# Kernel optimization log

Hardware: AMD Instinct MI355X
Metric: run time of the kernel (lower is better)

The kernel has to match this reference:

```python
import jax, jax.numpy as jnp
import numpy as np

EMBED_DIM = 384
HIDDEN_DIM = 512
CODEBOOK_SIZE = 256
NUM_QUANTIZERS = 4
COMMIT_WEIGHT = 0.25
BATCH = 65536


def setup_inputs() -> dict:
    key = jax.random.key(0)
    ks = jax.random.split(key, 10)
    s_in = 1.0 / np.sqrt(EMBED_DIM)
    s_h = 1.0 / np.sqrt(HIDDEN_DIM)
    return {
        "x": jax.random.normal(ks[0], (BATCH, EMBED_DIM), jnp.float32),
        "enc_w1": jax.random.uniform(ks[1], (EMBED_DIM, HIDDEN_DIM), jnp.float32, -s_in, s_in),
        "enc_b1": jnp.zeros((HIDDEN_DIM,), jnp.float32),
        "enc_w2": jax.random.uniform(ks[2], (HIDDEN_DIM, HIDDEN_DIM), jnp.float32, -s_h, s_h),
        "enc_b2": jnp.zeros((HIDDEN_DIM,), jnp.float32),
        "codebooks": jax.random.normal(ks[3], (NUM_QUANTIZERS, CODEBOOK_SIZE, HIDDEN_DIM), jnp.float32),
        "dec_w1": jax.random.uniform(ks[4], (HIDDEN_DIM, HIDDEN_DIM), jnp.float32, -s_h, s_h),
        "dec_b1": jnp.zeros((HIDDEN_DIM,), jnp.float32),
        "dec_w2": jax.random.uniform(ks[5], (HIDDEN_DIM, EMBED_DIM), jnp.float32, -s_h, s_h),
        "dec_b2": jnp.zeros((EMBED_DIM,), jnp.float32),
    }


def _residual_vq(z, codebooks):
    """Sequential residual VQ with straight-through estimator and commitment loss.
    z: [B, D]; codebooks: [Q, K, D]. Returns quantized [B, D], indices [B, Q], commit_loss scalar."""
    residual = z
    quantized_out = jnp.zeros_like(z)
    commit_loss = jnp.asarray(0.0, z.dtype)
    idx_list = []
    for q in range(NUM_QUANTIZERS):
        cb = codebooks[q]  # [K, D]
        # nearest code: argmin ||r - c||^2 == argmax (2 r.c - ||c||^2)
        scores = 2.0 * (residual @ cb.T) - jnp.sum(cb * cb, axis=-1)  # [B, K]
        idx = jnp.argmax(scores, axis=-1)  # [B]
        quant = cb[idx]  # [B, D] gather
        commit_loss = commit_loss + COMMIT_WEIGHT * jnp.mean(
            (residual - jax.lax.stop_gradient(quant)) ** 2)
        # straight-through: value = quant, gradient flows to residual
        quant_st = residual + jax.lax.stop_gradient(quant - residual)
        quantized_out = quantized_out + quant_st
        residual = residual - jax.lax.stop_gradient(quant)
        idx_list.append(idx)
    indices = jnp.stack(idx_list, axis=-1)  # [B, Q]
    return quantized_out, indices, commit_loss


def reference(x, enc_w1, enc_b1, enc_w2, enc_b2, codebooks,
              dec_w1, dec_b1, dec_w2, dec_b2):
    # encoder MLP
    z = jax.nn.relu(x @ enc_w1 + enc_b1) @ enc_w2 + enc_b2  # [B, H]
    quantized, indices, commit_loss = _residual_vq(z, codebooks)
    # decoder MLP
    recon = jax.nn.relu(quantized @ dec_w1 + dec_b1) @ dec_w2 + dec_b2  # [B, E]
    recon_loss = jnp.mean((recon - x) ** 2)
    return recon, indices, recon_loss, commit_loss
```

## Files before the change

### kernel.cpp

```cpp
#include <hip/hip_runtime.h>
#include <cfloat>
#include <cstddef>


#define BATCH   65536
#define EDIM    384
#define HDIM    512
#define NCODE   256
#define NQ      4

#define OUT_IDX_OFF 25165824
#define OUT_RL_OFF  25427968
#define WS_BUFA     0
#define WS_BUFB     33554432
#define WS_CBSPL    67108864
#define WS_CNORM    67633152
#define WS_COMMITP  67634176
#define WS_RECONP   67636224
#define WS_W1S      67637760
#define WS_W2S      67834368
#define WS_W3S      68096512
#define WS_W4S      68358656

typedef _Float16 half8 __attribute__((ext_vector_type(8)));
typedef float    f32x16 __attribute__((ext_vector_type(16)));

__device__ __forceinline__ void cvt_hl(const float4& a0, const float4& a1,
                                       half8& h, half8& l)
{
    float vs[8] = {a0.x, a0.y, a0.z, a0.w, a1.x, a1.y, a1.z, a1.w};
#pragma unroll
    for (int j = 0; j < 8; ++j) {
        _Float16 hv = (_Float16)vs[j];
        h[j] = hv;
        l[j] = (_Float16)(vs[j] - (float)hv);
    }
}

__global__ __launch_bounds__(256)
void split_w(const float* __restrict__ W, unsigned short* __restrict__ out,
             int N, int K)
{
    int u = blockIdx.x * 256 + threadIdx.x;
    int col  = u % N;
    int rem  = u / N;
    int khalf = rem & 1;
    int kt    = rem >> 1;
    int kbase = kt * 16 + khalf * 8;
    half8 h, l;
#pragma unroll
    for (int j = 0; j < 8; ++j) {
        float v = W[(size_t)(kbase + j) * N + col];
        _Float16 hv = (_Float16)v;
        h[j] = hv;
        l[j] = (_Float16)(v - (float)hv);
    }
    size_t eh = ((size_t)(kt * 4 + khalf)) * N + col;
    size_t el = ((size_t)(kt * 4 + 2 + khalf)) * N + col;
    *reinterpret_cast<half8*>(out + eh * 8) = h;
    *reinterpret_cast<half8*>(out + el * 8) = l;
}

template <int BN, bool RELU, bool LOSS>
__global__ __launch_bounds__(256, 2)
void gemm_reg(const float* __restrict__ A, const unsigned short* __restrict__ Wsp,
              const float* __restrict__ bias, float* __restrict__ C,
              const float* __restrict__ X, float* __restrict__ lossP,
              int N, int K)
{
    constexpr int WN = BN / 128;
    constexpr int WM = 4 / WN;
    constexpr int MR = 128 / WM;
    constexpr int FM = MR / 32;

    const int tid  = threadIdx.x;
    const int wid  = tid >> 6;
    const int lane = tid & 63;
    const int l31  = lane & 31;
    const int lh   = lane >> 5;
    const int wm   = wid / WN;
    const int wn   = wid % WN;
    const int row0 = blockIdx.y * 128;
    const int n0   = blockIdx.x * BN;
    const int nkt  = K / 16;

    f32x16 acc[FM][4];
#pragma unroll
    for (int m = 0; m < FM; ++m)
#pragma unroll
        for (int n = 0; n < 4; ++n) acc[m][n] = (f32x16)(0.0f);

    const float* ap[FM];
#pragma unroll
    for (int fm = 0; fm < FM; ++fm)
        ap[fm] = A + (size_t)(row0 + wm * MR + fm * 32 + l31) * K + lh * 8;

    const half8* b8 = reinterpret_cast<const half8*>(Wsp);
    const int colb = n0 + wn * 128 + l31;

#pragma unroll 2
    for (int kt = 0; kt < nkt; ++kt) {
        half8 Ah[FM], Al[FM];
#pragma unroll
        for (int fm = 0; fm < FM; ++fm) {
            float4 a0 = *reinterpret_cast<const float4*>(ap[fm] + kt * 16);
            float4 a1 = *reinterpret_cast<const float4*>(ap[fm] + kt * 16 + 4);
            cvt_hl(a0, a1, Ah[fm], Al[fm]);
        }
        const size_t eh = (size_t)(kt * 4 + lh) * N + colb;
        const size_t el = (size_t)(kt * 4 + 2 + lh) * N + colb;
#pragma unroll
        for (int nt = 0; nt < 4; ++nt) {
            half8 Bh = b8[eh + nt * 32];
            half8 Bl = b8[el + nt * 32];
#pragma unroll
            for (int fm = 0; fm < FM; ++fm) {
                acc[fm][nt] = __builtin_amdgcn_mfma_f32_32x32x16_f16(Ah[fm], Bh, acc[fm][nt], 0, 0, 0);
                acc[fm][nt] = __builtin_amdgcn_mfma_f32_32x32x16_f16(Ah[fm], Bl, acc[fm][nt], 0, 0, 0);
                acc[fm][nt] = __builtin_amdgcn_mfma_f32_32x32x16_f16(Al[fm], Bh, acc[fm][nt], 0, 0, 0);
            }
        }
    }

    float lacc = 0.f;
#pragma unroll
    for (int fm = 0; fm < FM; ++fm) {
#pragma unroll
        for (int nt = 0; nt < 4; ++nt) {
            const int col = n0 + wn * 128 + nt * 32 + l31;
            const float b = bias[col];
#pragma unroll
            for (int rg = 0; rg < 16; ++rg) {
                const int row = row0 + wm * MR + fm * 32 + (rg & 3) + 8 * (rg >> 2) + 4 * lh;
                float v = acc[fm][nt][rg] + b;
                if (RELU) v = v > 0.f ? v : 0.f;
                C[(size_t)row * N + col] = v;
                if constexpr (LOSS) {
                    float d = v - X[(size_t)row * N + col];
                    lacc = fmaf(d, d, lacc);
                }
            }
        }
    }

    if constexpr (LOSS) {
        __shared__ float red[256];
        red[tid] = lacc;
        __syncthreads();
        for (int s = 128; s > 0; s >>= 1) {
            if (tid < s) red[tid] += red[tid + s];
            __syncthreads();
        }
        if (tid == 0) lossP[blockIdx.y * gridDim.x + blockIdx.x] = red[0];
    }
}

__global__ __launch_bounds__(64)
void cnorm_kernel(const float* __restrict__ cb, float* __restrict__ cnorm)
{
    const int code = blockIdx.x;
    const int lane = threadIdx.x;
    const float* r = cb + (size_t)code * HDIM;
    float s = 0.f;
    for (int k = lane; k < HDIM; k += 64) s = fmaf(r[k], r[k], s);
#pragma unroll
    for (int off = 32; off > 0; off >>= 1) s += __shfl_down(s, off);
    if (lane == 0) cnorm[code] = s;
}

__global__ __launch_bounds__(256)
void split_cb(const float* __restrict__ cb, unsigned short* __restrict__ out)
{
    int u = blockIdx.x * 256 + threadIdx.x;
    int q    = u >> 14;
    int rem  = u & 16383;
    int code = rem >> 6;
    int kt   = (rem >> 1) & 31;
    int khalf = rem & 1;
    int k = kt * 16 + khalf * 8;
    const float* p = cb + ((size_t)(q * NCODE + code)) * HDIM + k;
    float4 v0 = *reinterpret_cast<const float4*>(p);
    float4 v1 = *reinterpret_cast<const float4*>(p + 4);
    half8 h, l;
    cvt_hl(v0, v1, h, l);
    size_t o = (size_t)(q * 32 + kt) * 8192 + (size_t)khalf * 2048 + (size_t)code * 8;
    *reinterpret_cast<half8*>(out + o)        = h;
    *reinterpret_cast<half8*>(out + o + 4096) = l;
}

template <bool LAST>
__global__ __launch_bounds__(256, 2)
void vq_stage(int q,
              const float* __restrict__ Rin, float* __restrict__ Rout,
              const float* __restrict__ zsrc,
              const unsigned short* __restrict__ cbs,
              const float* __restrict__ cb,
              const float* __restrict__ cnorm,
              float* __restrict__ idx_out,
              float* __restrict__ commitP)
{
    __shared__ float sval[2][128];
    __shared__ int   sidx[2][128];
    __shared__ int   idxbuf[128];
    __shared__ float red[256];

    const int tid  = threadIdx.x;
    const int wid  = tid >> 6;
    const int lane = tid & 63;
    const int l31  = lane & 31;
    const int lh   = lane >> 5;
    const int wm   = wid >> 1;
    const int wn   = wid & 1;
    const int row0 = blockIdx.x * 128;

    f32x16 acc[2][4];
#pragma unroll
    for (int m = 0; m < 2; ++m)
#pragma unroll
        for (int n = 0; n < 4; ++n) acc[m][n] = (f32x16)(0.0f);

    const float* ap[2];
#pragma unroll
    for (int fm = 0; fm < 2; ++fm)
        ap[fm] = Rin + (size_t)(row0 + wm * 64 + fm * 32 + l31) * HDIM + lh * 8;

    const half8* c8 = reinterpret_cast<const half8*>(cbs);
    const size_t qbase = (size_t)q * 32 * 1024;
    const int code_b = wn * 128 + l31;

#pragma unroll 4
    for (int kt = 0; kt < 32; ++kt) {
        half8 Ah[2], Al[2];
#pragma unroll
        for (int fm = 0; fm < 2; ++fm) {
            float4 a0 = *reinterpret_cast<const float4*>(ap[fm] + kt * 16);
            float4 a1 = *reinterpret_cast<const float4*>(ap[fm] + kt * 16 + 4);
            cvt_hl(a0, a1, Ah[fm], Al[fm]);
        }
        const size_t eh = qbase + (size_t)kt * 1024 + (size_t)lh * 256 + code_b;
#pragma unroll
        for (int nt = 0; nt < 4; ++nt) {
            half8 Bh = c8[eh + nt * 32];
            half8 Bl = c8[eh + 512 + nt * 32];
#pragma unroll
            for (int fm = 0; fm < 2; ++fm) {
                acc[fm][nt] = __builtin_amdgcn_mfma_f32_32x32x16_f16(Ah[fm], Bh, acc[fm][nt], 0, 0, 0);
                acc[fm][nt] = __builtin_amdgcn_mfma_f32_32x32x16_f16(Ah[fm], Bl, acc[fm][nt], 0, 0, 0);
                acc[fm][nt] = __builtin_amdgcn_mfma_f32_32x32x16_f16(Al[fm], Bh, acc[fm][nt], 0, 0, 0);
            }
        }
    }

    const float* cn = cnorm + q * NCODE;
#pragma unroll
    for (int Mt = 0; Mt < 2; ++Mt) {
#pragma unroll
        for (int rg = 0; rg < 16; ++rg) {
            float bv = -FLT_MAX;
            int   bi = 0;
#pragma unroll
            for (int nt = 0; nt < 4; ++nt) {
                const int code = wn * 128 + nt * 32 + l31;
                float s = 2.f * acc[Mt][nt][rg] - cn[code];
                if (s > bv || (s == bv && code < bi)) { bv = s; bi = code; }
            }
#pragma unroll
            for (int m = 1; m < 32; m <<= 1) {
                float ov = __shfl_xor(bv, m, 64);
                int   oi = __shfl_xor(bi, m, 64);
                if (ov > bv || (ov == bv && oi < bi)) { bv = ov; bi = oi; }
            }
            if (l31 == 0) {
                int row = wm * 64 + Mt * 32 + (rg & 3) + 8 * (rg >> 2) + 4 * lh;
                sval[wn][row] = bv;
                sidx[wn][row] = bi;
            }
        }
    }
    __syncthreads();
    if (tid < 128) {
        float v0 = sval[0][tid], v1 = sval[1][tid];
        int   i0 = sidx[0][tid], i1 = sidx[1][tid];
        int b = (v1 > v0 || (v1 == v0 && i1 < i0)) ? i1 : i0;
        idxbuf[tid] = b;
        idx_out[(size_t)(row0 + tid) * NQ + q] = (float)b;
    }
    __syncthreads();

    float ca = 0.f;
    const int rgrp = tid >> 3;
    const int lpos = tid & 7;
#pragma unroll
    for (int rr = 0; rr < 4; ++rr) {
        const int row = rr * 32 + rgrp;
        const float* rin  = Rin + (size_t)(row0 + row) * HDIM;
        const float* crow = cb + ((size_t)q * NCODE + idxbuf[row]) * HDIM;
        float* rout = Rout + (size_t)(row0 + row) * HDIM;
        const float* zr = LAST ? (zsrc + (size_t)(row0 + row) * HDIM) : nullptr;
#pragma unroll
        for (int j = 0; j < 16; ++j) {
            const int f4 = lpos + j * 8;
            float4 rv = *reinterpret_cast<const float4*>(rin + f4 * 4);
            float4 cv = *reinterpret_cast<const float4*>(crow + f4 * 4);
            float4 d;
            d.x = rv.x - cv.x; d.y = rv.y - cv.y;
            d.z = rv.z - cv.z; d.w = rv.w - cv.w;
            ca = fmaf(d.x, d.x, ca); ca = fmaf(d.y, d.y, ca);
            ca = fmaf(d.z, d.z, ca); ca = fmaf(d.w, d.w, ca);
            if constexpr (LAST) {
                float4 zv = *reinterpret_cast<const float4*>(zr + f4 * 4);
                float4 qv;
                qv.x = zv.x - d.x; qv.y = zv.y - d.y;
                qv.z = zv.z - d.z; qv.w = zv.w - d.w;
                *reinterpret_cast<float4*>(rout + f4 * 4) = qv;
            } else {
                *reinterpret_cast<float4*>(rout + f4 * 4) = d;
            }
        }
    }

    red[tid] = ca;
    __syncthreads();
    for (int s = 128; s > 0; s >>= 1) {
        if (tid < s) red[tid] += red[tid + s];
        __syncthreads();
    }
    if (tid == 0) commitP[q * 512 + blockIdx.x] = red[0];
}

__global__ __launch_bounds__(256)
void loss_reduce(const float* __restrict__ cP, int nc,
                 const float* __restrict__ rP, int nr,
                 float* __restrict__ out2)
{
    __shared__ float red[256];
    const int tid = threadIdx.x;

    float s = 0.f;
    for (int i = tid; i < nc; i += 256) s += cP[i];
    red[tid] = s;
    __syncthreads();
    for (int st = 128; st > 0; st >>= 1) {
        if (tid < st) red[tid] += red[tid + st];
        __syncthreads();
    }
    float ctot = red[0];
    __syncthreads();

    s = 0.f;
    for (int i = tid; i < nr; i += 256) s += rP[i];
    red[tid] = s;
    __syncthreads();
    for (int st = 128; st > 0; st >>= 1) {
        if (tid < st) red[tid] += red[tid + st];
        __syncthreads();
    }
    if (tid == 0) {
        out2[0] = red[0] / ((float)BATCH * (float)EDIM);
        out2[1] = 0.25f * ctot / ((float)BATCH * (float)HDIM);
    }
}

extern "C" void kernel_launch(void* const* d_in, const int* in_sizes, int n_in,
                              void* d_out, int out_size, void* d_ws, size_t ws_size,
                              hipStream_t stream)
{
    const float* x   = (const float*)d_in[0];
    const float* ew1 = (const float*)d_in[1];
    const float* eb1 = (const float*)d_in[2];
    const float* ew2 = (const float*)d_in[3];
    const float* eb2 = (const float*)d_in[4];
    const float* cb  = (const float*)d_in[5];
    const float* dw1 = (const float*)d_in[6];
    const float* db1 = (const float*)d_in[7];
    const float* dw2 = (const float*)d_in[8];
    const float* db2 = (const float*)d_in[9];

    float* out  = (float*)d_out;
    float* ws   = (float*)d_ws;
    float* bufA = ws + WS_BUFA;
    float* bufB = ws + WS_BUFB;
    unsigned short* cbs = (unsigned short*)(ws + WS_CBSPL);
    float* cn   = ws + WS_CNORM;
    float* cP   = ws + WS_COMMITP;
    float* rP   = ws + WS_RECONP;
    unsigned short* w1s = (unsigned short*)(ws + WS_W1S);
    unsigned short* w2s = (unsigned short*)(ws + WS_W2S);
    unsigned short* w3s = (unsigned short*)(ws + WS_W3S);
    unsigned short* w4s = (unsigned short*)(ws + WS_W4S);

    cnorm_kernel<<<NQ * NCODE, 64, 0, stream>>>(cb, cn);
    split_cb<<<256, 256, 0, stream>>>(cb, cbs);
    split_w<<<(EDIM / 16) * 2 * HDIM / 256, 256, 0, stream>>>(ew1, w1s, HDIM, EDIM);
    split_w<<<(HDIM / 16) * 2 * HDIM / 256, 256, 0, stream>>>(ew2, w2s, HDIM, HDIM);
    split_w<<<(HDIM / 16) * 2 * HDIM / 256, 256, 0, stream>>>(dw1, w3s, HDIM, HDIM);
    split_w<<<(HDIM / 16) * 2 * EDIM / 256, 256, 0, stream>>>(dw2, w4s, EDIM, HDIM);

    gemm_reg<256, true, false><<<dim3(HDIM / 256, BATCH / 128), 256, 0, stream>>>(
        x, w1s, eb1, bufA, nullptr, nullptr, HDIM, EDIM);
    gemm_reg<256, false, false><<<dim3(HDIM / 256, BATCH / 128), 256, 0, stream>>>(
        bufA, w2s, eb2, bufB, nullptr, nullptr, HDIM, HDIM);

    float* idxo = out + OUT_IDX_OFF;
    vq_stage<false><<<512, 256, 0, stream>>>(0, bufB, bufA, nullptr, cbs, cb, cn, idxo, cP);
    vq_stage<false><<<512, 256, 0, stream>>>(1, bufA, bufA, nullptr, cbs, cb, cn, idxo, cP);
    vq_stage<false><<<512, 256, 0, stream>>>(2, bufA, bufA, nullptr, cbs, cb, cn, idxo, cP);
    vq_stage<true ><<<512, 256, 0, stream>>>(3, bufA, bufB, bufB,    cbs, cb, cn, idxo, cP);

    gemm_reg<256, true, false><<<dim3(HDIM / 256, BATCH / 128), 256, 0, stream>>>(
        bufB, w3s, db1, bufA, nullptr, nullptr, HDIM, HDIM);
    gemm_reg<128, false, true><<<dim3(EDIM / 128, BATCH / 128), 256, 0, stream>>>(
        bufA, w4s, db2, out, x, rP, EDIM, HDIM);

    loss_reduce<<<1, 256, 0, stream>>>(cP, NQ * 512, rP,
                                       (BATCH / 128) * (EDIM / 128),
                                       out + OUT_RL_OFF);
}
```

Baseline: 1.046 ms.

## Software-pipeline register prefetch of A and B tiles in GEMM and VQ kernels

Adds a register-level multi-stage prefetch to the GEMM and VQ-score kernels. A operands are loaded three k-steps ahead and B operands two k-steps ahead, with the K loop fully unrolled through a compile-time trip count. This is meant to hide global-memory latency behind the MFMA work. The extra buffers raise register pressure, so launch bounds drop to one block per SIMD, which lowers occupancy.

```diff
diff --git a/kernel.cpp b/kernel.cpp
--- a/kernel.cpp
+++ b/kernel.cpp
@@ -61,17 +61,20 @@
     *reinterpret_cast<half8*>(out + el * 8) = l;
 }
 
-template <int BN, bool RELU, bool LOSS>
-__global__ __launch_bounds__(256, 2)
+template <int BN, int NKT, bool RELU, bool LOSS>
+__global__ __launch_bounds__(256, 1)
 void gemm_reg(const float* __restrict__ A, const unsigned short* __restrict__ Wsp,
               const float* __restrict__ bias, float* __restrict__ C,
               const float* __restrict__ X, float* __restrict__ lossP,
-              int N, int K)
+              int N)
 {
     constexpr int WN = BN / 128;
     constexpr int WM = 4 / WN;
     constexpr int MR = 128 / WM;
     constexpr int FM = MR / 32;
+    constexpr int K  = NKT * 16;
+    constexpr int DA = 3;
+    constexpr int DB = 2;
 
     const int tid  = threadIdx.x;
     const int wid  = tid >> 6;
@@ -82,7 +85,6 @@
     const int wn   = wid % WN;
     const int row0 = blockIdx.y * 128;
     const int n0   = blockIdx.x * BN;
-    const int nkt  = K / 16;
 
     f32x16 acc[FM][4];
 #pragma unroll
@@ -98,28 +100,63 @@
     const half8* b8 = reinterpret_cast<const half8*>(Wsp);
     const int colb = n0 + wn * 128 + l31;
 
-#pragma unroll 2
-    for (int kt = 0; kt < nkt; ++kt) {
+    float4 ar0[DA][FM], ar1[DA][FM];
+    half8  brh[DB][4], brl[DB][4];
+
+#pragma unroll
+    for (int p = 0; p < DA; ++p)
+#pragma unroll
+        for (int fm = 0; fm < FM; ++fm) {
+            ar0[p][fm] = *reinterpret_cast<const float4*>(ap[fm] + p * 16);
+            ar1[p][fm] = *reinterpret_cast<const float4*>(ap[fm] + p * 16 + 4);
+        }
+#pragma unroll
+    for (int p = 0; p < DB; ++p) {
+        const size_t eh = (size_t)(p * 4 + lh) * N + colb;
+        const size_t el = (size_t)(p * 4 + 2 + lh) * N + colb;
+#pragma unroll
+        for (int nt = 0; nt < 4; ++nt) {
+            brh[p][nt] = b8[eh + nt * 32];
+            brl[p][nt] = b8[el + nt * 32];
+        }
+    }
+
+#pragma unroll
+    for (int kt = 0; kt < NKT; ++kt) {
+        const int sa = kt % DA;
+        const int sb = kt % DB;
+
         half8 Ah[FM], Al[FM];
 #pragma unroll
-        for (int fm = 0; fm < FM; ++fm) {
-            float4 a0 = *reinterpret_cast<const float4*>(ap[fm] + kt * 16);
-            float4 a1 = *reinterpret_cast<const float4*>(ap[fm] + kt * 16 + 4);
-            cvt_hl(a0, a1, Ah[fm], Al[fm]);
-        }
-        const size_t eh = (size_t)(kt * 4 + lh) * N + colb;
-        const size_t el = (size_t)(kt * 4 + 2 + lh) * N + colb;
-#pragma unroll
-        for (int nt = 0; nt < 4; ++nt) {
-            half8 Bh = b8[eh + nt * 32];
-            half8 Bl = b8[el + nt * 32];
+        for (int fm = 0; fm < FM; ++fm)
+            cvt_hl(ar0[sa][fm], ar1[sa][fm], Ah[fm], Al[fm]);
+        if (kt + DA < NKT) {
 #pragma unroll
             for (int fm = 0; fm < FM; ++fm) {
-                acc[fm][nt] = __builtin_amdgcn_mfma_f32_32x32x16_f16(Ah[fm], Bh, acc[fm][nt], 0, 0, 0);
-                acc[fm][nt] = __builtin_amdgcn_mfma_f32_32x32x16_f16(Ah[fm], Bl, acc[fm][nt], 0, 0, 0);
-                acc[fm][nt] = __builtin_amdgcn_mfma_f32_32x32x16_f16(Al[fm], Bh, acc[fm][nt], 0, 0, 0);
-            }
-        }
+                ar0[sa][fm] = *reinterpret_cast<const float4*>(ap[fm] + (kt + DA) * 16);
+                ar1[sa][fm] = *reinterpret_cast<const float4*>(ap[fm] + (kt + DA) * 16 + 4);
+            }
+        }
+        half8 Bh[4], Bl[4];
+#pragma unroll
+        for (int nt = 0; nt < 4; ++nt) { Bh[nt] = brh[sb][nt]; Bl[nt] = brl[sb][nt]; }
+        if (kt + DB < NKT) {
+            const size_t eh = (size_t)((kt + DB) * 4 + lh) * N + colb;
+            const size_t el = (size_t)((kt + DB) * 4 + 2 + lh) * N + colb;
+#pragma unroll
+            for (int nt = 0; nt < 4; ++nt) {
+                brh[sb][nt] = b8[eh + nt * 32];
+                brl[sb][nt] = b8[el + nt * 32];
+            }
+        }
+#pragma unroll
+        for (int nt = 0; nt < 4; ++nt)
+#pragma unroll
+            for (int fm = 0; fm < FM; ++fm) {
+                acc[fm][nt] = __builtin_amdgcn_mfma_f32_32x32x16_f16(Ah[fm], Bh[nt], acc[fm][nt], 0, 0, 0);
+                acc[fm][nt] = __builtin_amdgcn_mfma_f32_32x32x16_f16(Ah[fm], Bl[nt], acc[fm][nt], 0, 0, 0);
+                acc[fm][nt] = __builtin_amdgcn_mfma_f32_32x32x16_f16(Al[fm], Bh[nt], acc[fm][nt], 0, 0, 0);
+            }
     }
 
     float lacc = 0.f;
@@ -189,7 +226,7 @@
 }
 
 template <bool LAST>
-__global__ __launch_bounds__(256, 2)
+__global__ __launch_bounds__(256, 1)
 void vq_stage(int q,
               const float* __restrict__ Rin, float* __restrict__ Rout,
               const float* __restrict__ zsrc,
@@ -199,6 +236,10 @@
               float* __restrict__ idx_out,
               float* __restrict__ commitP)
 {
+    constexpr int DA = 3;
+    constexpr int DB = 2;
+    constexpr int NKT = 32;
+
     __shared__ float sval[2][128];
     __shared__ int   sidx[2][128];
     __shared__ int   idxbuf[128];
@@ -228,27 +269,61 @@
     const size_t qbase = (size_t)q * 32 * 1024;
     const int code_b = wn * 128 + l31;
 
-#pragma unroll 4
-    for (int kt = 0; kt < 32; ++kt) {
+    float4 ar0[DA][2], ar1[DA][2];
+    half8  brh[DB][4], brl[DB][4];
+
+#pragma unroll
+    for (int p = 0; p < DA; ++p)
+#pragma unroll
+        for (int fm = 0; fm < 2; ++fm) {
+            ar0[p][fm] = *reinterpret_cast<const float4*>(ap[fm] + p * 16);
+            ar1[p][fm] = *reinterpret_cast<const float4*>(ap[fm] + p * 16 + 4);
+        }
+#pragma unroll
+    for (int p = 0; p < DB; ++p) {
+        const size_t eh = qbase + (size_t)p * 1024 + (size_t)lh * 256 + code_b;
+#pragma unroll
+        for (int nt = 0; nt < 4; ++nt) {
+            brh[p][nt] = c8[eh + nt * 32];
+            brl[p][nt] = c8[eh + 512 + nt * 32];
+        }
+    }
+
+#pragma unroll
+    for (int kt = 0; kt < NKT; ++kt) {
+        const int sa = kt % DA;
+        const int sb = kt % DB;
+
         half8 Ah[2], Al[2];
 #pragma unroll
-        for (int fm = 0; fm < 2; ++fm) {
-            float4 a0 = *reinterpret_cast<const float4*>(ap[fm] + kt * 16);
-            float4 a1 = *reinterpret_cast<const float4*>(ap[fm] + kt * 16 + 4);
-            cvt_hl(a0, a1, Ah[fm], Al[fm]);
-        }
-        const size_t eh = qbase + (size_t)kt * 1024 + (size_t)lh * 256 + code_b;
-#pragma unroll
-        for (int nt = 0; nt < 4; ++nt) {
-            half8 Bh = c8[eh + nt * 32];
-            half8 Bl = c8[eh + 512 + nt * 32];
+        for (int fm = 0; fm < 2; ++fm)
+            cvt_hl(ar0[sa][fm], ar1[sa][fm], Ah[fm], Al[fm]);
+        if (kt + DA < NKT) {
 #pragma unroll
             for (int fm = 0; fm < 2; ++fm) {
-                acc[fm][nt] = __builtin_amdgcn_mfma_f32_32x32x16_f16(Ah[fm], Bh, acc[fm][nt], 0, 0, 0);
-                acc[fm][nt] = __builtin_amdgcn_mfma_f32_32x32x16_f16(Ah[fm], Bl, acc[fm][nt], 0, 0, 0);
-                acc[fm][nt] = __builtin_amdgcn_mfma_f32_32x32x16_f16(Al[fm], Bh, acc[fm][nt], 0, 0, 0);
-            }
-        }
+                ar0[sa][fm] = *reinterpret_cast<const float4*>(ap[fm] + (kt + DA) * 16);
+                ar1[sa][fm] = *reinterpret_cast<const float4*>(ap[fm] + (kt + DA) * 16 + 4);
+            }
+        }
+        half8 Bh[4], Bl[4];
+#pragma unroll
+        for (int nt = 0; nt < 4; ++nt) { Bh[nt] = brh[sb][nt]; Bl[nt] = brl[sb][nt]; }
+        if (kt + DB < NKT) {
+            const size_t eh = qbase + (size_t)(kt + DB) * 1024 + (size_t)lh * 256 + code_b;
+#pragma unroll
+            for (int nt = 0; nt < 4; ++nt) {
+                brh[sb][nt] = c8[eh + nt * 32];
+                brl[sb][nt] = c8[eh + 512 + nt * 32];
+            }
+        }
+#pragma unroll
+        for (int nt = 0; nt < 4; ++nt)
+#pragma unroll
+            for (int fm = 0; fm < 2; ++fm) {
+                acc[fm][nt] = __builtin_amdgcn_mfma_f32_32x32x16_f16(Ah[fm], Bh[nt], acc[fm][nt], 0, 0, 0);
+                acc[fm][nt] = __builtin_amdgcn_mfma_f32_32x32x16_f16(Ah[fm], Bl[nt], acc[fm][nt], 0, 0, 0);
+                acc[fm][nt] = __builtin_amdgcn_mfma_f32_32x32x16_f16(Al[fm], Bh[nt], acc[fm][nt], 0, 0, 0);
+            }
     }
 
     const float* cn = cnorm + q * NCODE;
@@ -396,10 +471,10 @@
     split_w<<<(HDIM / 16) * 2 * HDIM / 256, 256, 0, stream>>>(dw1, w3s, HDIM, HDIM);
     split_w<<<(HDIM / 16) * 2 * EDIM / 256, 256, 0, stream>>>(dw2, w4s, EDIM, HDIM);
 
-    gemm_reg<256, true, false><<<dim3(HDIM / 256, BATCH / 128), 256, 0, stream>>>(
-        x, w1s, eb1, bufA, nullptr, nullptr, HDIM, EDIM);
-    gemm_reg<256, false, false><<<dim3(HDIM / 256, BATCH / 128), 256, 0, stream>>>(
-        bufA, w2s, eb2, bufB, nullptr, nullptr, HDIM, HDIM);
+    gemm_reg<256, 24, true, false><<<dim3(HDIM / 256, BATCH / 128), 256, 0, stream>>>(
+        x, w1s, eb1, bufA, nullptr, nullptr, HDIM);
+    gemm_reg<256, 32, false, false><<<dim3(HDIM / 256, BATCH / 128), 256, 0, stream>>>(
+        bufA, w2s, eb2, bufB, nullptr, nullptr, HDIM);
 
     float* idxo = out + OUT_IDX_OFF;
     vq_stage<false><<<512, 256, 0, stream>>>(0, bufB, bufA, nullptr, cbs, cb, cn, idxo, cP);
@@ -407,10 +482,10 @@
     vq_stage<false><<<512, 256, 0, stream>>>(2, bufA, bufA, nullptr, cbs, cb, cn, idxo, cP);
     vq_stage<true ><<<512, 256, 0, stream>>>(3, bufA, bufB, bufB,    cbs, cb, cn, idxo, cP);
 
-    gemm_reg<256, true, false><<<dim3(HDIM / 256, BATCH / 128), 256, 0, stream>>>(
-        bufB, w3s, db1, bufA, nullptr, nullptr, HDIM, HDIM);
-    gemm_reg<128, false, true><<<dim3(EDIM / 128, BATCH / 128), 256, 0, stream>>>(
-        bufA, w4s, db2, out, x, rP, EDIM, HDIM);
+    gemm_reg<256, 32, true, false><<<dim3(HDIM / 256, BATCH / 128), 256, 0, stream>>>(
+        bufB, w3s, db1, bufA, nullptr, nullptr, HDIM);
+    gemm_reg<128, 32, false, true><<<dim3(EDIM / 128, BATCH / 128), 256, 0, stream>>>(
+        bufA, w4s, db2, out, x, rP, EDIM);
 
     loss_reduce<<<1, 256, 0, stream>>>(cP, NQ * 512, rP,
                                        (BATCH / 128) * (EDIM / 128),
```

Measured after the change: 1.220 ms. 1.17x slower.

## Pipeline GEMM and VQ tiles through LDS with pre-split fp16 hi/lo activations

Applied to the files above, without the earlier changes.

Replaces direct global loads in the GEMM and VQ kernels with a three-buffer LDS pipeline filled by global_load_lds, using manual vmcnt waits and raw barriers. Intermediate activations are now stored already split into fp16 hi/lo pairs in a k-tiled layout, and a new split_x kernel pre-splits the input x. The aim is to hide global memory latency and to stop every output-column block from redoing the fp32-to-fp16 split of the same activations. The cost is an extra pass over x and hand-written wait counts and buffer indexing that must match exactly, plus LDS use that may lower occupancy.

```diff
diff --git a/kernel.cpp b/kernel.cpp
--- a/kernel.cpp
+++ b/kernel.cpp
@@ -1,6 +1,7 @@
 #include <hip/hip_runtime.h>
 #include <cfloat>
 #include <cstddef>
+#include <cstdint>
 
 
 #define BATCH   65536
@@ -11,8 +12,8 @@
 
 #define OUT_IDX_OFF 25165824
 #define OUT_RL_OFF  25427968
-#define WS_BUFA     0
-#define WS_BUFB     33554432
+#define WS_P0       0
+#define WS_P1       33554432
 #define WS_CBSPL    67108864
 #define WS_CNORM    67633152
 #define WS_COMMITP  67634176
@@ -25,16 +26,53 @@
 typedef _Float16 half8 __attribute__((ext_vector_type(8)));
 typedef float    f32x16 __attribute__((ext_vector_type(16)));
 
-__device__ __forceinline__ void cvt_hl(const float4& a0, const float4& a1,
-                                       half8& h, half8& l)
-{
-    float vs[8] = {a0.x, a0.y, a0.z, a0.w, a1.x, a1.y, a1.z, a1.w};
+__device__ __forceinline__ void cvt_hl8(const float* vs, half8& h, half8& l)
+{
 #pragma unroll
     for (int j = 0; j < 8; ++j) {
         _Float16 hv = (_Float16)vs[j];
         h[j] = hv;
         l[j] = (_Float16)(vs[j] - (float)hv);
     }
+}
+
+__device__ __forceinline__ void gll16(const unsigned short* g, unsigned short* l)
+{
+    __builtin_amdgcn_global_load_lds(
+        (const __attribute__((address_space(1))) unsigned int*)g,
+        (__attribute__((address_space(3))) unsigned int*)l, 16, 0, 0);
+}
+
+template <int N> __device__ __forceinline__ void waitvm()
+{
+    __builtin_amdgcn_sched_barrier(0);
+    if constexpr (N == 0)      asm volatile("s_waitcnt vmcnt(0)" ::: "memory");
+    else if constexpr (N == 4) asm volatile("s_waitcnt vmcnt(4)" ::: "memory");
+    else if constexpr (N == 6) asm volatile("s_waitcnt vmcnt(6)" ::: "memory");
+    __builtin_amdgcn_sched_barrier(0);
+}
+__device__ __forceinline__ void barrier_raw()
+{
+    __builtin_amdgcn_s_barrier();
+    __builtin_amdgcn_sched_barrier(0);
+}
+
+__global__ __launch_bounds__(256)
+void split_x(const float* __restrict__ x, unsigned short* __restrict__ xs)
+{
+    int u = blockIdx.x * 256 + threadIdx.x;
+    int row = u / 48;
+    int rem = u % 48;
+    int kt = rem >> 1, khalf = rem & 1;
+    const float* p = x + (size_t)row * EDIM + kt * 16 + khalf * 8;
+    float vs[8];
+#pragma unroll
+    for (int j = 0; j < 8; ++j) vs[j] = p[j];
+    half8 h, l;
+    cvt_hl8(vs, h, l);
+    unsigned short* o = xs + (size_t)row * 768 + kt * 32 + khalf * 8;
+    *reinterpret_cast<half8*>(o)      = h;
+    *reinterpret_cast<half8*>(o + 16) = l;
 }
 
 __global__ __launch_bounds__(256)
@@ -47,31 +85,67 @@
     int khalf = rem & 1;
     int kt    = rem >> 1;
     int kbase = kt * 16 + khalf * 8;
+    float vs[8];
+#pragma unroll
+    for (int j = 0; j < 8; ++j) vs[j] = W[(size_t)(kbase + j) * N + col];
     half8 h, l;
-#pragma unroll
-    for (int j = 0; j < 8; ++j) {
-        float v = W[(size_t)(kbase + j) * N + col];
-        _Float16 hv = (_Float16)v;
-        h[j] = hv;
-        l[j] = (_Float16)(v - (float)hv);
-    }
-    size_t eh = ((size_t)(kt * 4 + khalf)) * N + col;
-    size_t el = ((size_t)(kt * 4 + 2 + khalf)) * N + col;
-    *reinterpret_cast<half8*>(out + eh * 8) = h;
-    *reinterpret_cast<half8*>(out + el * 8) = l;
-}
-
-template <int BN, bool RELU, bool LOSS>
+    cvt_hl8(vs, h, l);
+    *reinterpret_cast<half8*>(out + ((size_t)(kt * 4 + khalf) * N + col) * 8)     = h;
+    *reinterpret_cast<half8*>(out + ((size_t)(kt * 4 + 2 + khalf) * N + col) * 8) = l;
+}
+
+__global__ __launch_bounds__(256)
+void split_cb(const float* __restrict__ cb, unsigned short* __restrict__ out)
+{
+    int u = blockIdx.x * 256 + threadIdx.x;
+    int q    = u >> 14;
+    int rem  = u & 16383;
+    int code = rem >> 6;
+    int kt   = (rem >> 1) & 31;
+    int khalf = rem & 1;
+    int k = kt * 16 + khalf * 8;
+    const float* p = cb + ((size_t)(q * NCODE + code)) * HDIM + k;
+    float vs[8];
+#pragma unroll
+    for (int j = 0; j < 8; ++j) vs[j] = p[j];
+    half8 h, l;
+    cvt_hl8(vs, h, l);
+    size_t o = (size_t)(q * 32 + kt) * 8192 + (size_t)khalf * 2048 + (size_t)code * 8;
+    *reinterpret_cast<half8*>(out + o)        = h;
+    *reinterpret_cast<half8*>(out + o + 4096) = l;
+}
+
+__global__ __launch_bounds__(64)
+void cnorm_kernel(const float* __restrict__ cb, float* __restrict__ cnorm)
+{
+    const int code = blockIdx.x;
+    const int lane = threadIdx.x;
+    const float* r = cb + (size_t)code * HDIM;
+    float s = 0.f;
+    for (int k = lane; k < HDIM; k += 64) s = fmaf(r[k], r[k], s);
+#pragma unroll
+    for (int off = 32; off > 0; off >>= 1) s += __shfl_down(s, off);
+    if (lane == 0) cnorm[code] = s;
+}
+
+template <int BN, int NKT, int OMODE, bool RELU>
 __global__ __launch_bounds__(256, 2)
-void gemm_reg(const float* __restrict__ A, const unsigned short* __restrict__ Wsp,
-              const float* __restrict__ bias, float* __restrict__ C,
-              const float* __restrict__ X, float* __restrict__ lossP,
-              int N, int K)
-{
-    constexpr int WN = BN / 128;
-    constexpr int WM = 4 / WN;
-    constexpr int MR = 128 / WM;
-    constexpr int FM = MR / 32;
+void gemm_pl(const unsigned short* __restrict__ Ain,
+             const unsigned short* __restrict__ Wsp,
+             const float* __restrict__ bias, void* __restrict__ Cout,
+             const float* __restrict__ X, float* __restrict__ lossP, int N)
+{
+    constexpr int WN  = BN / 128;
+    constexpr int WM  = 4 / WN;
+    constexpr int MR  = 128 / WM;
+    constexpr int FM  = MR / 32;
+    constexpr int K   = NKT * 16;
+    constexpr int BOFF = 4096;
+    constexpr int BUFU = 4096 + 4 * BN * 8;
+    constexpr int NIB = BN / 64;
+    constexpr int GPI = 2 + NIB;
+
+    __shared__ __align__(16) unsigned short lds[3][BUFU];
 
     const int tid  = threadIdx.x;
     const int wid  = tid >> 6;
@@ -82,7 +156,6 @@
     const int wn   = wid % WN;
     const int row0 = blockIdx.y * 128;
     const int n0   = blockIdx.x * BN;
-    const int nkt  = K / 16;
 
     f32x16 acc[FM][4];
 #pragma unroll
@@ -90,29 +163,42 @@
 #pragma unroll
         for (int n = 0; n < 4; ++n) acc[m][n] = (f32x16)(0.0f);
 
-    const float* ap[FM];
-#pragma unroll
-    for (int fm = 0; fm < FM; ++fm)
-        ap[fm] = A + (size_t)(row0 + wm * MR + fm * 32 + l31) * K + lh * 8;
-
-    const half8* b8 = reinterpret_cast<const half8*>(Wsp);
-    const int colb = n0 + wn * 128 + l31;
-
-#pragma unroll 2
-    for (int kt = 0; kt < nkt; ++kt) {
+    auto stageB = [&](int buf, int kt) {
+        const unsigned short* img = Wsp + (size_t)kt * 4 * N * 8;
+        unsigned short* dstb = &lds[buf][BOFF];
+#pragma unroll
+        for (int t = 0; t < NIB; ++t) {
+            int e = (wid * NIB + t) * 64 + lane;
+            int u = (BN == 256) ? (e >> 8) : (e >> 7);
+            int c = e & (BN - 1);
+            gll16(img + ((size_t)u * N + n0 + c) * 8, dstb + (size_t)e * 8);
+        }
+    };
+    auto stageA = [&](int buf, int kt) {
+#pragma unroll
+        for (int t = 0; t < 2; ++t) {
+            int i = wid * 2 + t;
+            int u = i >> 1, rh = i & 1;
+            int row = rh * 64 + lane;
+            gll16(Ain + (size_t)(row0 + row) * (2 * K) + kt * 32 + u * 8,
+                  &lds[buf][(size_t)i * 512 + (size_t)lane * 8]);
+        }
+    };
+    auto compute = [&](int buf) {
+        const unsigned short* Ab = &lds[buf][0];
+        const unsigned short* Bb = &lds[buf][BOFF];
         half8 Ah[FM], Al[FM];
 #pragma unroll
         for (int fm = 0; fm < FM; ++fm) {
-            float4 a0 = *reinterpret_cast<const float4*>(ap[fm] + kt * 16);
-            float4 a1 = *reinterpret_cast<const float4*>(ap[fm] + kt * 16 + 4);
-            cvt_hl(a0, a1, Ah[fm], Al[fm]);
-        }
-        const size_t eh = (size_t)(kt * 4 + lh) * N + colb;
-        const size_t el = (size_t)(kt * 4 + 2 + lh) * N + colb;
+            int row = wm * MR + fm * 32 + l31;
+            Ah[fm] = *reinterpret_cast<const half8*>(Ab + (size_t)lh * 1024 + (size_t)row * 8);
+            Al[fm] = *reinterpret_cast<const half8*>(Ab + (size_t)(2 + lh) * 1024 + (size_t)row * 8);
+        }
 #pragma unroll
         for (int nt = 0; nt < 4; ++nt) {
-            half8 Bh = b8[eh + nt * 32];
-            half8 Bl = b8[el + nt * 32];
+            int col = wn * 128 + nt * 32 + l31;
+            half8 Bh = *reinterpret_cast<const half8*>(Bb + (size_t)lh * BN * 8 + (size_t)col * 8);
+            half8 Bl = *reinterpret_cast<const half8*>(Bb + (size_t)(2 + lh) * BN * 8 + (size_t)col * 8);
 #pragma unroll
             for (int fm = 0; fm < FM; ++fm) {
                 acc[fm][nt] = __builtin_amdgcn_mfma_f32_32x32x16_f16(Ah[fm], Bh, acc[fm][nt], 0, 0, 0);
@@ -120,30 +206,64 @@
                 acc[fm][nt] = __builtin_amdgcn_mfma_f32_32x32x16_f16(Al[fm], Bh, acc[fm][nt], 0, 0, 0);
             }
         }
-    }
-
-    float lacc = 0.f;
-#pragma unroll
-    for (int fm = 0; fm < FM; ++fm) {
-#pragma unroll
-        for (int nt = 0; nt < 4; ++nt) {
-            const int col = n0 + wn * 128 + nt * 32 + l31;
-            const float b = bias[col];
-#pragma unroll
-            for (int rg = 0; rg < 16; ++rg) {
-                const int row = row0 + wm * MR + fm * 32 + (rg & 3) + 8 * (rg >> 2) + 4 * lh;
-                float v = acc[fm][nt][rg] + b;
-                if (RELU) v = v > 0.f ? v : 0.f;
-                C[(size_t)row * N + col] = v;
-                if constexpr (LOSS) {
+    };
+
+    stageA(0, 0); stageB(0, 0);
+    stageA(1, 1); stageB(1, 1);
+    waitvm<GPI>();
+    barrier_raw();
+    for (int kt = 0; kt < NKT; ++kt) {
+        const int cur = kt % 3;
+        if (kt + 2 < NKT) { const int nb = (kt + 2) % 3; stageA(nb, kt + 2); stageB(nb, kt + 2); }
+        compute(cur);
+        if (kt < NKT - 2) waitvm<GPI>(); else waitvm<0>();
+        barrier_raw();
+    }
+
+    if constexpr (OMODE == 0) {
+        unsigned short* o = (unsigned short*)Cout;
+        const size_t rs = (size_t)N * 2;
+#pragma unroll
+        for (int fm = 0; fm < FM; ++fm) {
+#pragma unroll
+            for (int nt = 0; nt < 4; ++nt) {
+                const int col = n0 + wn * 128 + nt * 32 + l31;
+                const float b = bias[col];
+                const size_t cbo = (size_t)(col >> 4) * 32 + (size_t)((col >> 3) & 1) * 8 + (col & 7);
+#pragma unroll
+                for (int rg = 0; rg < 16; ++rg) {
+                    const int row = row0 + wm * MR + fm * 32 + (rg & 3) + 8 * (rg >> 2) + 4 * lh;
+                    float v = acc[fm][nt][rg] + b;
+                    if (RELU) v = v > 0.f ? v : 0.f;
+                    _Float16 hv = (_Float16)v;
+                    _Float16 lv = (_Float16)(v - (float)hv);
+                    union { _Float16 f; unsigned short u; } ch, cl;
+                    ch.f = hv; cl.f = lv;
+                    o[(size_t)row * rs + cbo]      = ch.u;
+                    o[(size_t)row * rs + cbo + 16] = cl.u;
+                }
+            }
+        }
+    } else {
+        float* C = (float*)Cout;
+        float lacc = 0.f;
+#pragma unroll
+        for (int fm = 0; fm < FM; ++fm) {
+#pragma unroll
+            for (int nt = 0; nt < 4; ++nt) {
+                const int col = n0 + wn * 128 + nt * 32 + l31;
+                const float b = bias[col];
+#pragma unroll
+                for (int rg = 0; rg < 16; ++rg) {
+                    const int row = row0 + wm * MR + fm * 32 + (rg & 3) + 8 * (rg >> 2) + 4 * lh;
+                    float v = acc[fm][nt][rg] + b;
+                    if (RELU) v = v > 0.f ? v : 0.f;
+                    C[(size_t)row * N + col] = v;
                     float d = v - X[(size_t)row * N + col];
                     lacc = fmaf(d, d, lacc);
                 }
             }
         }
-    }
-
-    if constexpr (LOSS) {
         __shared__ float red[256];
         red[tid] = lacc;
         __syncthreads();
@@ -155,50 +275,19 @@
     }
 }
 
-__global__ __launch_bounds__(64)
-void cnorm_kernel(const float* __restrict__ cb, float* __restrict__ cnorm)
-{
-    const int code = blockIdx.x;
-    const int lane = threadIdx.x;
-    const float* r = cb + (size_t)code * HDIM;
-    float s = 0.f;
-    for (int k = lane; k < HDIM; k += 64) s = fmaf(r[k], r[k], s);
-#pragma unroll
-    for (int off = 32; off > 0; off >>= 1) s += __shfl_down(s, off);
-    if (lane == 0) cnorm[code] = s;
-}
-
-__global__ __launch_bounds__(256)
-void split_cb(const float* __restrict__ cb, unsigned short* __restrict__ out)
-{
-    int u = blockIdx.x * 256 + threadIdx.x;
-    int q    = u >> 14;
-    int rem  = u & 16383;
-    int code = rem >> 6;
-    int kt   = (rem >> 1) & 31;
-    int khalf = rem & 1;
-    int k = kt * 16 + khalf * 8;
-    const float* p = cb + ((size_t)(q * NCODE + code)) * HDIM + k;
-    float4 v0 = *reinterpret_cast<const float4*>(p);
-    float4 v1 = *reinterpret_cast<const float4*>(p + 4);
-    half8 h, l;
-    cvt_hl(v0, v1, h, l);
-    size_t o = (size_t)(q * 32 + kt) * 8192 + (size_t)khalf * 2048 + (size_t)code * 8;
-    *reinterpret_cast<half8*>(out + o)        = h;
-    *reinterpret_cast<half8*>(out + o + 4096) = l;
-}
-
 template <bool LAST>
 __global__ __launch_bounds__(256, 2)
 void vq_stage(int q,
-              const float* __restrict__ Rin, float* __restrict__ Rout,
-              const float* __restrict__ zsrc,
+              const unsigned short* __restrict__ Rin, unsigned short* __restrict__ Rout,
+              const unsigned short* __restrict__ zsrc,
               const unsigned short* __restrict__ cbs,
               const float* __restrict__ cb,
               const float* __restrict__ cnorm,
               float* __restrict__ idx_out,
               float* __restrict__ commitP)
 {
+    constexpr int NKT = 32;
+    __shared__ __align__(16) unsigned short lds[3][12288];
     __shared__ float sval[2][128];
     __shared__ int   sidx[2][128];
     __shared__ int   idxbuf[128];
@@ -219,29 +308,40 @@
 #pragma unroll
         for (int n = 0; n < 4; ++n) acc[m][n] = (f32x16)(0.0f);
 
-    const float* ap[2];
-#pragma unroll
-    for (int fm = 0; fm < 2; ++fm)
-        ap[fm] = Rin + (size_t)(row0 + wm * 64 + fm * 32 + l31) * HDIM + lh * 8;
-
-    const half8* c8 = reinterpret_cast<const half8*>(cbs);
-    const size_t qbase = (size_t)q * 32 * 1024;
-    const int code_b = wn * 128 + l31;
-
-#pragma unroll 4
-    for (int kt = 0; kt < 32; ++kt) {
+    auto stageA = [&](int buf, int kt) {
+#pragma unroll
+        for (int t = 0; t < 2; ++t) {
+            int i = wid * 2 + t;
+            int u = i >> 1, rh = i & 1;
+            int row = rh * 64 + lane;
+            gll16(Rin + (size_t)(row0 + row) * 1024 + kt * 32 + u * 8,
+                  &lds[buf][(size_t)i * 512 + (size_t)lane * 8]);
+        }
+    };
+    auto stageB = [&](int buf, int kt) {
+        const unsigned short* img = cbs + (size_t)(q * 32 + kt) * 8192;
+        unsigned short* dstb = &lds[buf][4096];
+#pragma unroll
+        for (int t = 0; t < 4; ++t) {
+            int e = (wid * 4 + t) * 64 + lane;
+            gll16(img + (size_t)e * 8, dstb + (size_t)e * 8);
+        }
+    };
+    auto compute = [&](int buf) {
+        const unsigned short* Ab = &lds[buf][0];
+        const unsigned short* Bb = &lds[buf][4096];
         half8 Ah[2], Al[2];
 #pragma unroll
         for (int fm = 0; fm < 2; ++fm) {
-            float4 a0 = *reinterpret_cast<const float4*>(ap[fm] + kt * 16);
-            float4 a1 = *reinterpret_cast<const float4*>(ap[fm] + kt * 16 + 4);
-            cvt_hl(a0, a1, Ah[fm], Al[fm]);
-        }
-        const size_t eh = qbase + (size_t)kt * 1024 + (size_t)lh * 256 + code_b;
+            int row = wm * 64 + fm * 32 + l31;
+            Ah[fm] = *reinterpret_cast<const half8*>(Ab + (size_t)lh * 1024 + (size_t)row * 8);
+            Al[fm] = *reinterpret_cast<const half8*>(Ab + (size_t)(2 + lh) * 1024 + (size_t)row * 8);
+        }
 #pragma unroll
         for (int nt = 0; nt < 4; ++nt) {
-            half8 Bh = c8[eh + nt * 32];
-            half8 Bl = c8[eh + 512 + nt * 32];
+            int col = wn * 128 + nt * 32 + l31;
+            half8 Bh = *reinterpret_cast<const half8*>(Bb + (size_t)lh * 2048 + (size_t)col * 8);
+            half8 Bl = *reinterpret_cast<const half8*>(Bb + (size_t)(2 + lh) * 2048 + (size_t)col * 8);
 #pragma unroll
             for (int fm = 0; fm < 2; ++fm) {
                 acc[fm][nt] = __builtin_amdgcn_mfma_f32_32x32x16_f16(Ah[fm], Bh, acc[fm][nt], 0, 0, 0);
@@ -249,6 +349,18 @@
                 acc[fm][nt] = __builtin_amdgcn_mfma_f32_32x32x16_f16(Al[fm], Bh, acc[fm][nt], 0, 0, 0);
             }
         }
+    };
+
+    stageA(0, 0); stageB(0, 0);
+    stageA(1, 1); stageB(1, 1);
+    waitvm<6>();
+    barrier_raw();
+    for (int kt = 0; kt < NKT; ++kt) {
+        const int cur = kt % 3;
+        if (kt + 2 < NKT) { const int nb = (kt + 2) % 3; stageA(nb, kt + 2); stageB(nb, kt + 2); }
+        compute(cur);
+        if (kt < NKT - 2) waitvm<6>(); else waitvm<0>();
+        barrier_raw();
     }
 
     const float* cn = cnorm + q * NCODE;
@@ -293,29 +405,41 @@
 #pragma unroll
     for (int rr = 0; rr < 4; ++rr) {
         const int row = rr * 32 + rgrp;
-        const float* rin  = Rin + (size_t)(row0 + row) * HDIM;
+        const unsigned short* rip = Rin + (size_t)(row0 + row) * 1024;
+        unsigned short*       rop = Rout + (size_t)(row0 + row) * 1024;
         const float* crow = cb + ((size_t)q * NCODE + idxbuf[row]) * HDIM;
-        float* rout = Rout + (size_t)(row0 + row) * HDIM;
-        const float* zr = LAST ? (zsrc + (size_t)(row0 + row) * HDIM) : nullptr;
-#pragma unroll
-        for (int j = 0; j < 16; ++j) {
-            const int f4 = lpos + j * 8;
-            float4 rv = *reinterpret_cast<const float4*>(rin + f4 * 4);
-            float4 cv = *reinterpret_cast<const float4*>(crow + f4 * 4);
-            float4 d;
-            d.x = rv.x - cv.x; d.y = rv.y - cv.y;
-            d.z = rv.z - cv.z; d.w = rv.w - cv.w;
-            ca = fmaf(d.x, d.x, ca); ca = fmaf(d.y, d.y, ca);
-            ca = fmaf(d.z, d.z, ca); ca = fmaf(d.w, d.w, ca);
+        const unsigned short* zp = LAST ? (zsrc + (size_t)(row0 + row) * 1024) : nullptr;
+#pragma unroll
+        for (int j = 0; j < 8; ++j) {
+            const int g = lpos + j * 8;
+            const size_t off = (size_t)(g >> 1) * 32 + (size_t)(g & 1) * 8;
+            half8 rh = *reinterpret_cast<const half8*>(rip + off);
+            half8 rl = *reinterpret_cast<const half8*>(rip + off + 16);
+            float4 c0 = *reinterpret_cast<const float4*>(crow + g * 8);
+            float4 c1 = *reinterpret_cast<const float4*>(crow + g * 8 + 4);
+            float cv[8] = {c0.x, c0.y, c0.z, c0.w, c1.x, c1.y, c1.z, c1.w};
+            half8 zh, zl;
             if constexpr (LAST) {
-                float4 zv = *reinterpret_cast<const float4*>(zr + f4 * 4);
-                float4 qv;
-                qv.x = zv.x - d.x; qv.y = zv.y - d.y;
-                qv.z = zv.z - d.z; qv.w = zv.w - d.w;
-                *reinterpret_cast<float4*>(rout + f4 * 4) = qv;
-            } else {
-                *reinterpret_cast<float4*>(rout + f4 * 4) = d;
-            }
+                zh = *reinterpret_cast<const half8*>(zp + off);
+                zl = *reinterpret_cast<const half8*>(zp + off + 16);
+            }
+            half8 oh, ol;
+#pragma unroll
+            for (int e = 0; e < 8; ++e) {
+                float rv = (float)rh[e] + (float)rl[e];
+                float d = rv - cv[e];
+                ca = fmaf(d, d, ca);
+                float ov = d;
+                if constexpr (LAST) {
+                    float zv = (float)zh[e] + (float)zl[e];
+                    ov = zv - d;
+                }
+                _Float16 hv = (_Float16)ov;
+                oh[e] = hv;
+                ol[e] = (_Float16)(ov - (float)hv);
+            }
+            *reinterpret_cast<half8*>(rop + off)      = oh;
+            *reinterpret_cast<half8*>(rop + off + 16) = ol;
         }
     }
 
@@ -376,14 +500,15 @@
     const float* dw2 = (const float*)d_in[8];
     const float* db2 = (const float*)d_in[9];
 
-    float* out  = (float*)d_out;
-    float* ws   = (float*)d_ws;
-    float* bufA = ws + WS_BUFA;
-    float* bufB = ws + WS_BUFB;
+    float* out = (float*)d_out;
+    float* ws  = (float*)d_ws;
+    unsigned short* P0  = (unsigned short*)(ws + WS_P0);
+    unsigned short* P1  = (unsigned short*)(ws + WS_P1);
+    unsigned short* XS  = P1;
     unsigned short* cbs = (unsigned short*)(ws + WS_CBSPL);
-    float* cn   = ws + WS_CNORM;
-    float* cP   = ws + WS_COMMITP;
-    float* rP   = ws + WS_RECONP;
+    float* cn = ws + WS_CNORM;
+    float* cP = ws + WS_COMMITP;
+    float* rP = ws + WS_RECONP;
     unsigned short* w1s = (unsigned short*)(ws + WS_W1S);
     unsigned short* w2s = (unsigned short*)(ws + WS_W2S);
     unsigned short* w3s = (unsigned short*)(ws + WS_W3S);
@@ -391,26 +516,27 @@
 
     cnorm_kernel<<<NQ * NCODE, 64, 0, stream>>>(cb, cn);
     split_cb<<<256, 256, 0, stream>>>(cb, cbs);
+    split_x<<<BATCH * 48 / 256, 256, 0, stream>>>(x, XS);
     split_w<<<(EDIM / 16) * 2 * HDIM / 256, 256, 0, stream>>>(ew1, w1s, HDIM, EDIM);
     split_w<<<(HDIM / 16) * 2 * HDIM / 256, 256, 0, stream>>>(ew2, w2s, HDIM, HDIM);
     split_w<<<(HDIM / 16) * 2 * HDIM / 256, 256, 0, stream>>>(dw1, w3s, HDIM, HDIM);
     split_w<<<(HDIM / 16) * 2 * EDIM / 256, 256, 0, stream>>>(dw2, w4s, EDIM, HDIM);
 
-    gemm_reg<256, true, false><<<dim3(HDIM / 256, BATCH / 128), 256, 0, stream>>>(
-        x, w1s, eb1, bufA, nullptr, nullptr, HDIM, EDIM);
-    gemm_reg<256, false, false><<<dim3(HDIM / 256, BATCH / 128), 256, 0, stream>>>(
-        bufA, w2s, eb2, bufB, nullptr, nullptr, HDIM, HDIM);
+    gemm_pl<256, 24, 0, true><<<dim3(HDIM / 256, BATCH / 128), 256, 0, stream>>>(
+        XS, w1s, eb1, P0, nullptr, nullptr, HDIM);
+    gemm_pl<256, 32, 0, false><<<dim3(HDIM / 256, BATCH / 128), 256, 0, stream>>>(
+        P0, w2s, eb2, P1, nullptr, nullptr, HDIM);
 
     float* idxo = out + OUT_IDX_OFF;
-    vq_stage<false><<<512, 256, 0, stream>>>(0, bufB, bufA, nullptr, cbs, cb, cn, idxo, cP);
-    vq_stage<false><<<512, 256, 0, stream>>>(1, bufA, bufA, nullptr, cbs, cb, cn, idxo, cP);
-    vq_stage<false><<<512, 256, 0, stream>>>(2, bufA, bufA, nullptr, cbs, cb, cn, idxo, cP);
-    vq_stage<true ><<<512, 256, 0, stream>>>(3, bufA, bufB, bufB,    cbs, cb, cn, idxo, cP);
-
-    gemm_reg<256, true, false><<<dim3(HDIM / 256, BATCH / 128), 256, 0, stream>>>(
-        bufB, w3s, db1, bufA, nullptr, nullptr, HDIM, HDIM);
-    gemm_reg<128, false, true><<<dim3(EDIM / 128, BATCH / 128), 256, 0, stream>>>(
-        bufA, w4s, db2, out, x, rP, EDIM, HDIM);
+    vq_stage<false><<<512, 256, 0, stream>>>(0, P1, P0, nullptr, cbs, cb, cn, idxo, cP);
+    vq_stage<false><<<512, 256, 0, stream>>>(1, P0, P0, nullptr, cbs, cb, cn, idxo, cP);
+    vq_stage<false><<<512, 256, 0, stream>>>(2, P0, P0, nullptr, cbs, cb, cn, idxo, cP);
+    vq_stage<true ><<<512, 256, 0, stream>>>(3, P0, P1, P1,      cbs, cb, cn, idxo, cP);
+
+    gemm_pl<256, 32, 0, true><<<dim3(HDIM / 256, BATCH / 128), 256, 0, stream>>>(
+        P1, w3s, db1, P0, nullptr, nullptr, HDIM);
+    gemm_pl<128, 32, 1, false><<<dim3(EDIM / 128, BATCH / 128), 256, 0, stream>>>(
+        P0, w4s, db2, out, x, rP, EDIM);
 
     loss_reduce<<<1, 256, 0, stream>>>(cP, NQ * 512, rP,
                                        (BATCH / 128) * (EDIM / 128),
```

Measured after the change: 989.6 us. 5.4% less time.
